# Optimization experiments

Measured on AMD Instinct MI355X. Metric: run time of the kernel, lower is better.

Reference implementation:

```python
import jax, jax.numpy as jnp
import numpy as np
import math

DIM = 2048; H = 16; QR = 1536; KVR = 512; DN = 128; DR = 64; DV = 128
BS = 4; S = 1024
QK_HEAD = DN + DR  # 192


def _rms(x, w, eps=1e-6):
    v = jnp.mean(x * x, axis=-1, keepdims=True)
    return w * (x * jax.lax.rsqrt(v + eps))


def _rope_cos_sin(seq_len, dim):
    inv_freq = 1.0 / (10000.0 ** (jnp.arange(0, dim, 2, dtype=jnp.float32) / dim))
    t = jnp.arange(seq_len, dtype=jnp.float32)
    freqs = jnp.einsum('s,d->sd', t, inv_freq)
    freqs = jnp.concatenate([freqs, freqs], axis=-1)  # [S, dim]
    return jnp.cos(freqs), jnp.sin(freqs)


def _rotate_half(x):
    x1, x2 = jnp.split(x, 2, axis=-1)
    return jnp.concatenate([-x2, x1], axis=-1)


def setup_inputs() -> dict:
    key = jax.random.key(0)
    ks = jax.random.split(key, 12)
    sd = 0.02
    x = jax.random.normal(ks[0], (BS, S, DIM), dtype=jnp.float32)
    # causal additive mask [b, s, t]
    i = jnp.arange(S)
    causal = jnp.where(i[:, None] >= i[None, :], 0.0, -1e9).astype(jnp.float32)
    mask = jnp.broadcast_to(causal, (BS, S, S))
    return {
        'x': x,
        'mask': mask,
        'wq_a_w': jax.random.normal(ks[1], (QR, DIM)) * sd,
        'wq_a_b': jnp.zeros((QR,), jnp.float32),
        'q_norm_w': jnp.ones((QR,), jnp.float32),
        'wq_b_w': jax.random.normal(ks[2], (H * QK_HEAD, QR)) * sd,
        'wq_b_b': jnp.zeros((H * QK_HEAD,), jnp.float32),
        'wkv_a_w': jax.random.normal(ks[3], (KVR + DR, DIM)) * sd,
        'wkv_a_b': jnp.zeros((KVR + DR,), jnp.float32),
        'kv_norm_w': jnp.ones((KVR,), jnp.float32),
        'wkv_b_w': jax.random.normal(ks[4], (H * (DN + DV), KVR)) * sd,
        'wo_w': jax.random.normal(ks[5], (DIM, H * DV)) * sd,
        'wo_b': jnp.zeros((DIM,), jnp.float32),
    }


def reference(x, mask, wq_a_w, wq_a_b, q_norm_w, wq_b_w, wq_b_b,
              wkv_a_w, wkv_a_b, kv_norm_w, wkv_b_w, wo_w, wo_b):
    bs, seq_len, _ = x.shape
    # Q low-rank path
    q = x @ wq_a_w.T + wq_a_b                     # [b,s,QR]
    q = _rms(q, q_norm_w)
    q = q @ wq_b_w.T + wq_b_b                     # [b,s,H*192]
    q = q.reshape(bs, seq_len, H, QK_HEAD)
    q_nope, q_pe = q[..., :DN], q[..., DN:]       # [b,s,h,128], [b,s,h,64]
    # compressed KV path
    kv = x @ wkv_a_w.T + wkv_a_b                  # [b,s,KVR+64]
    c, k_pe = kv[..., :KVR], kv[..., KVR:]        # [b,s,512], [b,s,64]
    # RoPE on the rope sub-dims
    cos, sin = _rope_cos_sin(seq_len, DR)         # [s,64]
    cos4 = cos[None, :, None, :]
    sin4 = sin[None, :, None, :]
    q_pe = q_pe * cos4 + _rotate_half(q_pe) * sin4
    k_pe4 = k_pe[:, :, None, :]
    k_pe = (k_pe4 * cos4 + _rotate_half(k_pe4) * sin4)[:, :, 0, :]  # [b,s,64]
    # weight absorption: wkv_b viewed [H, DN+DV, KVR]
    wkv_b = wkv_b_w.reshape(H, DN + DV, KVR)
    q_abs = jnp.einsum('bshd,hdc->bshc', q_nope, wkv_b[:, :DN])      # [b,s,h,512]
    c_n = _rms(c, kv_norm_w)                                         # [b,t,512]
    scores = (jnp.einsum('bshc,btc->bsht', q_abs, c_n)
              + jnp.einsum('bshr,btr->bsht', q_pe, k_pe)) / math.sqrt(QK_HEAD)
    scores = scores + mask[:, :, None, :]
    scores = jax.nn.softmax(scores, axis=-1)
    o = jnp.einsum('bsht,btc->bshc', scores, c_n)                    # [b,s,h,512]
    o = jnp.einsum('bshc,hdc->bshd', o, wkv_b[:, -DV:])              # [b,s,h,128]
    o = o.reshape(bs, seq_len, H * DV)
    return o @ wo_w.T + wo_b
```

## Files before the change

### kernel.cpp

```cpp
#include <hip/hip_runtime.h>


typedef __attribute__((ext_vector_type(8))) short bf16x8;
typedef __attribute__((ext_vector_type(4))) float f32x4;
typedef __attribute__((ext_vector_type(4))) int i32x4;
typedef unsigned short ushort_t;
typedef unsigned int uint32;

typedef const __attribute__((address_space(1))) void* gas_ptr;
typedef __attribute__((address_space(3))) void* las_ptr;

#define DEV __device__ __forceinline__
#define WAITVM(N) asm volatile("s_waitcnt vmcnt(" #N ")" ::: "memory")

DEV float b2f(ushort_t u) { return __uint_as_float(((uint32)u) << 16); }
DEV ushort_t f2b(float f) {
  uint32 u = __float_as_uint(f);
  return (ushort_t)((u + 0x7fffu + ((u >> 16) & 1u)) >> 16);
}
DEV uint32 pkb(float lo, float hi) { return (uint32)f2b(lo) | ((uint32)f2b(hi) << 16); }

DEV void c4seg(const float4* __restrict__ in, ushort4* __restrict__ out, int i, int n4) {
  if (i < n4) {
    float4 v = in[i];
    ushort4 o; o.x = f2b(v.x); o.y = f2b(v.y); o.z = f2b(v.z); o.w = f2b(v.w);
    out[i] = o;
  }
}
DEV void vbseg(const float* __restrict__ in, ushort_t* __restrict__ out, int i4, int dofs) {
  int c4 = i4 & 127, d = (i4 >> 7) & 127, h = i4 >> 14;
  const float4 v = *(const float4*)(in + ((long)(h * 256 + dofs + d)) * 512 + c4 * 4);
  ushort4 o; o.x = f2b(v.x); o.y = f2b(v.y); o.z = f2b(v.z); o.w = f2b(v.w);
  ((ushort4*)out)[i4] = o;
}
__global__ __launch_bounds__(256) void castall_k(
    const float* __restrict__ x, const float* __restrict__ wq_a_w,
    const float* __restrict__ wkv_a_w, const float* __restrict__ wq_b_w,
    const float* __restrict__ wo_w, const float* __restrict__ wkv_b_w,
    ushort_t* __restrict__ xb, ushort_t* __restrict__ wcomb,
    ushort_t* __restrict__ wqb, ushort_t* __restrict__ wo,
    ushort_t* __restrict__ wkvbv, ushort_t* __restrict__ wkvbn) {
  int blk = blockIdx.x, tid = threadIdx.x;
  if (blk < 8192) {
    c4seg((const float4*)x, (ushort4*)xb, blk * 256 + tid, 2097152);
  } else if (blk < 11264) {
    c4seg((const float4*)wq_a_w, (ushort4*)wcomb, (blk - 8192) * 256 + tid, 786432);
  } else if (blk < 12416) {
    c4seg((const float4*)wkv_a_w, (ushort4*)(wcomb + 1536 * 2048),
          (blk - 11264) * 256 + tid, 294912);
  } else if (blk < 17024) {
    c4seg((const float4*)wq_b_w, (ushort4*)wqb, (blk - 12416) * 256 + tid, 1179648);
  } else if (blk < 21120) {
    c4seg((const float4*)wo_w, (ushort4*)wo, (blk - 17024) * 256 + tid, 1048576);
  } else if (blk < 22144) {
    vbseg(wkv_b_w, wkvbv, (blk - 21120) * 256 + tid, 128);
  } else {
    vbseg(wkv_b_w, wkvbn, (blk - 22144) * 256 + tid, 0);
  }
}

DEV float block_reduce_sum(float v, float* sbuf) {
#pragma unroll
  for (int d = 32; d >= 1; d >>= 1) v += __shfl_xor(v, d);
  if ((threadIdx.x & 63) == 0) sbuf[threadIdx.x >> 6] = v;
  __syncthreads();
  return sbuf[0] + sbuf[1] + sbuf[2] + sbuf[3];
}

__global__ __launch_bounds__(256) void rms_1536_k(const float* __restrict__ in,
                                                  ushort_t* __restrict__ out,
                                                  const float* __restrict__ w) {
  __shared__ float sbuf[4];
  long row = blockIdx.x;
  const float* p = in + row * 1536;
  float v[6]; float ss = 0.f;
#pragma unroll
  for (int i = 0; i < 6; ++i) { v[i] = p[threadIdx.x + i * 256]; ss += v[i] * v[i]; }
  ss = block_reduce_sum(ss, sbuf);
  float sc = rsqrtf(ss * (1.0f / 1536.0f) + 1e-6f);
#pragma unroll
  for (int i = 0; i < 6; ++i) {
    int c = threadIdx.x + i * 256;
    out[row * 1536 + c] = f2b(v[i] * sc * w[c]);
  }
}

__global__ __launch_bounds__(512) void kvfuse_k(const float* __restrict__ kvf,
                                                const float* __restrict__ w,
                                                ushort_t* __restrict__ kcat,
                                                ushort_t* __restrict__ vtp,
                                                ushort_t* __restrict__ kabs) {
  __shared__ ushort_t sh[8 * 512];
  int tid = threadIdx.x, wv = tid >> 6, lane = tid & 63;
  long row = (long)blockIdx.x * 8 + wv;
  const float* p = kvf + row * 576;
  float4 v0 = *(const float4*)(p + lane * 8);
  float4 v1 = *(const float4*)(p + lane * 8 + 4);
  float ss = v0.x * v0.x + v0.y * v0.y + v0.z * v0.z + v0.w * v0.w
           + v1.x * v1.x + v1.y * v1.y + v1.z * v1.z + v1.w * v1.w;
#pragma unroll
  for (int d = 1; d <= 32; d <<= 1) ss += __shfl_xor(ss, d);
  float sc = rsqrtf(ss * (1.0f / 512.0f) + 1e-6f);
  float4 w0 = *(const float4*)(w + lane * 8);
  float4 w1 = *(const float4*)(w + lane * 8 + 4);
  ushort_t tmp[8];
  tmp[0] = f2b(v0.x * sc * w0.x); tmp[1] = f2b(v0.y * sc * w0.y);
  tmp[2] = f2b(v0.z * sc * w0.z); tmp[3] = f2b(v0.w * sc * w0.w);
  tmp[4] = f2b(v1.x * sc * w1.x); tmp[5] = f2b(v1.y * sc * w1.y);
  tmp[6] = f2b(v1.z * sc * w1.z); tmp[7] = f2b(v1.w * sc * w1.w);
  *(uint4*)(kcat + row * 576 + lane * 8) = *(uint4*)tmp;
  *(uint4*)(sh + wv * 512 + lane * 8) = *(uint4*)tmp;
  if (lane < 32) {
    int t = (int)(row & 1023);
    float x1 = p[512 + lane], x2 = p[544 + lane];
    float ang = (float)t * powf(10000.0f, -(float)lane * (1.0f / 32.0f));
    float s, c; sincosf(ang, &s, &c);
    ushort_t r1 = f2b(x1 * c - x2 * s), r2 = f2b(x2 * c + x1 * s);
    kcat[row * 576 + 512 + lane] = r1;
    kcat[row * 576 + 544 + lane] = r2;
#pragma unroll
    for (int h = 0; h < 16; ++h) {
      long base = ((long)h * 4096 + row) * 192;
      kabs[base + 128 + lane] = r1;
      kabs[base + 160 + lane] = r2;
    }
  }
  __syncthreads();
  ushort_t t8[8];
#pragma unroll
  for (int j = 0; j < 8; ++j) t8[j] = sh[j * 512 + tid];
  int b = blockIdx.x >> 7, tb = blockIdx.x & 127;
  *(uint4*)(vtp + (((long)b * 128 + tb) * 512 + tid) * 8) = *(uint4*)t8;
}

template <bool OUT_BF16>
__global__ __launch_bounds__(256) void gemm_bt_k(
    const ushort_t* __restrict__ A, int lda, long sAz,
    const ushort_t* __restrict__ B, int ldb, long sBz,
    void* __restrict__ C, int ldc, long sCz,
    const float* __restrict__ bias, float scale,
    int M, int N, int K) {
  __shared__ ushort_t As[2 * 4096];
  __shared__ ushort_t Bs[2 * 4096];
  int tid = threadIdx.x;
  int wave = tid >> 6, lane = tid & 63;
  int row0 = blockIdx.x * 128, col0 = blockIdx.y * 128;
  int z = blockIdx.z;
  const ushort_t* Az = A + (long)z * sAz;
  const ushort_t* Bz = B + (long)z * sBz;
  int wr = wave >> 1, wc = wave & 1;
  int lr = lane & 15, kq = lane >> 4;

  f32x4 acc[4][4];
#pragma unroll
  for (int m = 0; m < 4; ++m)
#pragma unroll
    for (int n = 0; n < 4; ++n) acc[m][n] = (f32x4){0.f, 0.f, 0.f, 0.f};

  auto stage = [&](int buf, int k0) {
#pragma unroll
    for (int rnd = 0; rnd < 2; ++rnd) {
      int e = rnd * 2048 + wave * 512 + lane * 8;
      int tr = e >> 5, tc = e & 31;
      int ar = row0 + tr; if (ar >= M) ar = M - 1;
      int br = col0 + tr; if (br >= N) br = N - 1;
      __builtin_amdgcn_global_load_lds((gas_ptr)(Az + (long)ar * lda + (k0 + tc)),
          (las_ptr)(As + buf * 4096 + rnd * 2048 + wave * 512), 16, 0, 0);
      __builtin_amdgcn_global_load_lds((gas_ptr)(Bz + (long)br * ldb + (k0 + tc)),
          (las_ptr)(Bs + buf * 4096 + rnd * 2048 + wave * 512), 16, 0, 0);
    }
  };

  stage(0, 0);
  int nk = K >> 5;
  for (int kt = 0; kt < nk; ++kt) {
    int cur = kt & 1;
    if (kt + 1 < nk) { stage(cur ^ 1, (kt + 1) * 32); WAITVM(4); }
    else { WAITVM(0); }
    __builtin_amdgcn_s_barrier();
    __builtin_amdgcn_sched_barrier(0);
    const ushort_t* Ac = As + cur * 4096;
    const ushort_t* Bc = Bs + cur * 4096;
    bf16x8 a[4], bb[4];
#pragma unroll
    for (int m = 0; m < 4; ++m)
      a[m] = *(const bf16x8*)(Ac + (wr * 64 + m * 16 + lr) * 32 + kq * 8);
#pragma unroll
    for (int n = 0; n < 4; ++n)
      bb[n] = *(const bf16x8*)(Bc + (wc * 64 + n * 16 + lr) * 32 + kq * 8);
#pragma unroll
    for (int m = 0; m < 4; ++m)
#pragma unroll
      for (int n = 0; n < 4; ++n)
        acc[m][n] = __builtin_amdgcn_mfma_f32_16x16x32_bf16(a[m], bb[n], acc[m][n], 0, 0, 0);
    __builtin_amdgcn_s_barrier();
  }

#pragma unroll
  for (int n = 0; n < 4; ++n) {
    int gcol = col0 + wc * 64 + n * 16 + lr;
    if (gcol >= N) continue;
    float bv = bias ? bias[gcol] : 0.f;
#pragma unroll
    for (int m = 0; m < 4; ++m) {
      int gr0 = row0 + wr * 64 + m * 16 + kq * 4;
#pragma unroll
      for (int r = 0; r < 4; ++r) {
        int gr = gr0 + r;
        if (gr < M) {
          float v = acc[m][n][r] * scale + bv;
          long ci = (long)z * sCz + (long)gr * ldc + gcol;
          if constexpr (OUT_BF16) ((ushort_t*)C)[ci] = f2b(v);
          else ((float*)C)[ci] = v;
        }
      }
    }
  }
}

template <int MODE>
__global__ __launch_bounds__(256) void gemm64_k(
    const ushort_t* __restrict__ A, int lda,
    const ushort_t* __restrict__ B, int ldb,
    void* __restrict__ C, int ldc,
    const float* __restrict__ bias,
    void* __restrict__ C2, const float* __restrict__ bias2,
    int M, int N, int K) {
  __shared__ ushort_t As[2 * 8192];
  __shared__ ushort_t Bs[2 * 8192];
  int tid = threadIdx.x;
  int wave = tid >> 6, lane = tid & 63;
  int row0 = blockIdx.x * 128, col0 = blockIdx.y * 128;
  int wr = wave >> 1, wc = wave & 1;
  int lr = lane & 15, kq = lane >> 4;
  int rsw = lr & 7;

  f32x4 acc[4][4];
#pragma unroll
  for (int m = 0; m < 4; ++m)
#pragma unroll
    for (int n = 0; n < 4; ++n) acc[m][n] = (f32x4){0.f, 0.f, 0.f, 0.f};

  auto stage = [&](int buf, int k0) {
#pragma unroll
    for (int ii = 0; ii < 4; ++ii) {
      int e = ii * 256 + tid;
      int r = e >> 3, c = e & 7;
      int scol = ((c ^ (r & 7)) << 3);
      int ar = row0 + r; if (ar >= M) ar = M - 1;
      int br = col0 + r; if (br >= N) br = N - 1;
      __builtin_amdgcn_global_load_lds((gas_ptr)(A + (long)ar * lda + k0 + scol),
          (las_ptr)(As + buf * 8192 + e * 8), 16, 0, 0);
      __builtin_amdgcn_global_load_lds((gas_ptr)(B + (long)br * ldb + k0 + scol),
          (las_ptr)(Bs + buf * 8192 + e * 8), 16, 0, 0);
    }
  };

  stage(0, 0);
  int nk = K >> 6;
  for (int kt = 0; kt < nk; ++kt) {
    int cur = kt & 1;
    if (kt + 1 < nk) { stage(cur ^ 1, (kt + 1) * 64); WAITVM(8); }
    else { WAITVM(0); }
    __builtin_amdgcn_s_barrier();
    __builtin_amdgcn_sched_barrier(0);
    const ushort_t* Ac = As + cur * 8192;
    const ushort_t* Bc = Bs + cur * 8192;
#pragma unroll
    for (int ks = 0; ks < 2; ++ks) {
      bf16x8 a[4], bb[4];
#pragma unroll
      for (int m = 0; m < 4; ++m) {
        int row = wr * 64 + m * 16 + lr;
        a[m] = *(const bf16x8*)(Ac + row * 64 + ((((ks << 2) | kq) ^ rsw) << 3));
      }
#pragma unroll
      for (int n = 0; n < 4; ++n) {
        int row = wc * 64 + n * 16 + lr;
        bb[n] = *(const bf16x8*)(Bc + row * 64 + ((((ks << 2) | kq) ^ rsw) << 3));
      }
#pragma unroll
      for (int m = 0; m < 4; ++m)
#pragma unroll
        for (int n = 0; n < 4; ++n)
          acc[m][n] = __builtin_amdgcn_mfma_f32_16x16x32_bf16(a[m], bb[n], acc[m][n], 0, 0, 0);
    }
    __builtin_amdgcn_s_barrier();
  }

  if constexpr (MODE == 0) {
#pragma unroll
    for (int n = 0; n < 4; ++n) {
      int gcol = col0 + wc * 64 + n * 16 + lr;
      if (gcol >= N) continue;
      float bv = bias[gcol];
#pragma unroll
      for (int m = 0; m < 4; ++m) {
        int gr0 = row0 + wr * 64 + m * 16 + kq * 4;
#pragma unroll
        for (int r = 0; r < 4; ++r) {
          int gr = gr0 + r;
          if (gr < M) ((float*)C)[(long)gr * ldc + gcol] = acc[m][n][r] + bv;
        }
      }
    }
  } else if constexpr (MODE == 1) {
#pragma unroll
    for (int n = 0; n < 4; ++n) {
      int gcol = col0 + wc * 64 + n * 16 + lr;
      if (gcol >= N) continue;
      if (gcol < 1536) {
        float bv = bias[gcol];
#pragma unroll
        for (int m = 0; m < 4; ++m) {
          int gr0 = row0 + wr * 64 + m * 16 + kq * 4;
#pragma unroll
          for (int r = 0; r < 4; ++r) {
            int gr = gr0 + r;
            ((float*)C)[(long)gr * 1536 + gcol] = acc[m][n][r] + bv;
          }
        }
      } else {
        int c2 = gcol - 1536;
        float bv = bias2[c2];
#pragma unroll
        for (int m = 0; m < 4; ++m) {
          int gr0 = row0 + wr * 64 + m * 16 + kq * 4;
#pragma unroll
          for (int r = 0; r < 4; ++r) {
            int gr = gr0 + r;
            ((float*)C2)[(long)gr * 576 + c2] = acc[m][n][r] + bv;
          }
        }
      }
    }
  } else {
    const float RS = 0.07216878364870322f;
    ushort_t* qc = (ushort_t*)C;
#pragma unroll
    for (int n = 0; n < 4; ++n) {
      int j = col0 + wc * 64 + n * 16 + lr;
      int h = j / 192, d = j - h * 192;
      if (d < 128) {
        float bv = bias[j];
#pragma unroll
        for (int m = 0; m < 4; ++m) {
          int gr0 = row0 + wr * 64 + m * 16 + kq * 4;
#pragma unroll
          for (int r = 0; r < 4; ++r) {
            int gr = gr0 + r;
            qc[((long)h * 4096 + gr) * 192 + d] = f2b((acc[m][n][r] + bv) * RS);
          }
        }
      } else if (d < 160) {
        int jj = d - 128;
        float bv1 = bias[j], bv2 = bias[j + 32];
        float invf = powf(10000.0f, -(float)jj * (1.0f / 32.0f));
#pragma unroll
        for (int m = 0; m < 4; ++m) {
          int gr0 = row0 + wr * 64 + m * 16 + kq * 4;
#pragma unroll
          for (int r = 0; r < 4; ++r) {
            int gr = gr0 + r;
            int t = gr & 1023;
            float s, c; sincosf((float)t * invf, &s, &c);
            float x1 = acc[m][n][r] + bv1;
            float x2 = acc[m][n + 2][r] + bv2;
            long base = ((long)h * 4096 + gr) * 192;
            qc[base + d] = f2b((x1 * c - x2 * s) * RS);
            qc[base + d + 32] = f2b((x2 * c + x1 * s) * RS);
          }
        }
      }
    }
  }
}

__global__ __launch_bounds__(512, 1) void flash5_k(const ushort_t* __restrict__ qcat2,
                                                   const ushort_t* __restrict__ kabs,
                                                   const ushort_t* __restrict__ vtp,
                                                   ushort_t* __restrict__ O) {
  __shared__ __align__(16) ushort_t SMEM[2 * 6400 + 2 * 16384];

  int tid = threadIdx.x;
  int wave = tid >> 6, lane = tid & 63;
  int lr = lane & 15, kq = lane >> 4;
  int bi = blockIdx.x;
  int jz = bi >> 6;
  int qb = (jz < 4) ? jz : 11 - jz;
  int bh = bi & 63;
  int h = bh >> 2, b = bh & 3;
  int s0 = qb * 128;
  int nt = (qb + 1) * 4;

  const ushort_t* kt = kabs + ((long)h * 4096 + b * 1024) * 192;
  const ushort_t* vt = vtp + (long)b * 524288;
  const ushort_t* qp = qcat2 + ((long)(h * 4096 + b * 1024 + s0 + wave * 16 + lr)) * 192 + kq * 8;

  auto stageK = [&](int buf, int t0) {
    const ushort_t* sb = kt + (long)t0 * 192;
    ushort_t* kb = SMEM + buf * 6400;
#pragma unroll
    for (int ii = 0; ii < 2; ++ii) {
      int c = ii * 512 + tid;
      if (ii == 1 && tid >= 288) break;
      int t = (int)((unsigned)c / 25u);
      int r = c - t * 25;
      int rr = (r == 24) ? 0 : r;
      const ushort_t* src = sb + t * 192 + rr * 8;
      __builtin_amdgcn_global_load_lds((gas_ptr)src, (las_ptr)(kb + c * 8), 16, 0, 0);
    }
  };
  auto stageV = [&](int buf, int t0) {
    const ushort_t* sb = vt + (long)(t0 >> 3) * 4096;
    ushort_t* vb = SMEM + 12800 + buf * 16384;
#pragma unroll
    for (int ii = 0; ii < 4; ++ii) {
      int c0 = (ii * 8 + wave) * 64;
      const ushort_t* src = sb + (long)(c0 + lane) * 8;
      __builtin_amdgcn_global_load_lds((gas_ptr)src, (las_ptr)(vb + c0 * 8), 16, 0, 0);
    }
  };

  stageK(0, 0); stageV(0, 0);
  bf16x8 qreg[6];
#pragma unroll
  for (int st = 0; st < 6; ++st) qreg[st] = *(const bf16x8*)(qp + st * 32);

  f32x4 o[32];
#pragma unroll
  for (int v = 0; v < 32; ++v) o[v] = (f32x4){0.f, 0.f, 0.f, 0.f};
  float m_run = -1e30f, l_run = 0.f;

  int row_g = s0 + wave * 16 + lr;
  int idx_lo = (((kq & 1) << 5) + lr) << 2;
  int idx_hi = idx_lo + 64;
  bool losel = (kq < 2);

  __syncthreads();

  for (int it = 0; it < nt; ++it) {
    int cur = it & 1;
    if (it + 1 < nt) { stageK(cur ^ 1, (it + 1) * 32); stageV(cur ^ 1, (it + 1) * 32); }
    const ushort_t* Kc = SMEM + cur * 6400;
    f32x4 sv0 = (f32x4){0.f, 0.f, 0.f, 0.f}, sv1 = sv0;
    __builtin_amdgcn_s_setprio(1);
#pragma unroll
    for (int st = 0; st < 6; ++st) {
      int off = st * 32 + kq * 8;
      bf16x8 k0 = *(const bf16x8*)(Kc + lr * 200 + off);
      bf16x8 k1 = *(const bf16x8*)(Kc + (16 + lr) * 200 + off);
      sv0 = __builtin_amdgcn_mfma_f32_16x16x32_bf16(k0, qreg[st], sv0, 0, 0, 0);
      sv1 = __builtin_amdgcn_mfma_f32_16x16x32_bf16(k1, qreg[st], sv1, 0, 0, 0);
    }
    __builtin_amdgcn_s_setprio(0);
    int t0 = it * 32;
    if (t0 >= s0) {
#pragma unroll
      for (int rr = 0; rr < 4; ++rr) {
        if (t0 + kq * 4 + rr > row_g) sv0[rr] = -1e30f;
        if (t0 + 16 + kq * 4 + rr > row_g) sv1[rr] = -1e30f;
      }
    }
    float mx = fmaxf(fmaxf(fmaxf(sv0[0], sv0[1]), fmaxf(sv0[2], sv0[3])),
                     fmaxf(fmaxf(sv1[0], sv1[1]), fmaxf(sv1[2], sv1[3])));
    mx = fmaxf(mx, __shfl_xor(mx, 16));
    mx = fmaxf(mx, __shfl_xor(mx, 32));
    float mn = (mx > m_run + 8.0f) ? mx : m_run;
    float alpha = __expf(m_run - mn);
    float p0 = __expf(sv0[0] - mn), p1 = __expf(sv0[1] - mn);
    float p2 = __expf(sv0[2] - mn), p3 = __expf(sv0[3] - mn);
    float p4 = __expf(sv1[0] - mn), p5 = __expf(sv1[1] - mn);
    float p6 = __expf(sv1[2] - mn), p7 = __expf(sv1[3] - mn);
    float psum = ((p0 + p1) + (p2 + p3)) + ((p4 + p5) + (p6 + p7));
    psum += __shfl_xor(psum, 16);
    psum += __shfl_xor(psum, 32);
    l_run = l_run * alpha + psum;
    m_run = mn;
    int u0 = (int)pkb(p0, p1), u1 = (int)pkb(p2, p3);
    int u2 = (int)pkb(p4, p5), u3 = (int)pkb(p6, p7);
    int b00 = __builtin_amdgcn_ds_bpermute(idx_lo, u0);
    int b10 = __builtin_amdgcn_ds_bpermute(idx_lo, u1);
    int b20 = __builtin_amdgcn_ds_bpermute(idx_lo, u2);
    int b30 = __builtin_amdgcn_ds_bpermute(idx_lo, u3);
    int b01 = __builtin_amdgcn_ds_bpermute(idx_hi, u0);
    int b11 = __builtin_amdgcn_ds_bpermute(idx_hi, u1);
    int b21 = __builtin_amdgcn_ds_bpermute(idx_hi, u2);
    int b31 = __builtin_amdgcn_ds_bpermute(idx_hi, u3);
    i32x4 w;
    w.x = losel ? b00 : b20; w.y = losel ? b10 : b30;
    w.z = losel ? b01 : b21; w.w = losel ? b11 : b31;
    bf16x8 pa = __builtin_bit_cast(bf16x8, w);
    float a0 = __shfl(alpha, kq * 4 + 0), a1 = __shfl(alpha, kq * 4 + 1);
    float a2 = __shfl(alpha, kq * 4 + 2), a3 = __shfl(alpha, kq * 4 + 3);
    if (__any((a0 != 1.f) | (a1 != 1.f) | (a2 != 1.f) | (a3 != 1.f))) {
      f32x4 av; av[0] = a0; av[1] = a1; av[2] = a2; av[3] = a3;
#pragma unroll
      for (int v = 0; v < 32; ++v) o[v] *= av;
    }
    const ushort_t* Vc = SMEM + 12800 + cur * 16384 + (kq * 512 + lr) * 8;
    __builtin_amdgcn_s_setprio(1);
#pragma unroll
    for (int v = 0; v < 32; ++v) {
      bf16x8 bv = *(const bf16x8*)(Vc + v * 128);
      o[v] = __builtin_amdgcn_mfma_f32_16x16x32_bf16(pa, bv, o[v], 0, 0, 0);
    }
    __builtin_amdgcn_s_setprio(0);
    __syncthreads();
  }
  float l0 = __shfl(l_run, kq * 4 + 0), l1 = __shfl(l_run, kq * 4 + 1);
  float l2 = __shfl(l_run, kq * 4 + 2), l3 = __shfl(l_run, kq * 4 + 3);
  f32x4 inv; inv[0] = 1.f / l0; inv[1] = 1.f / l1; inv[2] = 1.f / l2; inv[3] = 1.f / l3;
  ushort_t* ob = O + ((long)(h * 4096 + b * 1024 + s0 + wave * 16 + kq * 4)) * 512 + lr;
#pragma unroll
  for (int rr = 0; rr < 4; ++rr) {
    ushort_t* orow = ob + (long)rr * 512;
#pragma unroll
    for (int v = 0; v < 32; ++v) orow[v * 16] = f2b(o[v][rr] * inv[rr]);
  }
}

extern "C" void kernel_launch(void* const* d_in, const int* in_sizes, int n_in,
                              void* d_out, int out_size, void* d_ws, size_t ws_size,
                              hipStream_t stream) {
  (void)in_sizes; (void)n_in;
  const float* x         = (const float*)d_in[0];
  const float* wq_a_w    = (const float*)d_in[2];
  const float* wq_a_b    = (const float*)d_in[3];
  const float* q_norm_w  = (const float*)d_in[4];
  const float* wq_b_w    = (const float*)d_in[5];
  const float* wq_b_b    = (const float*)d_in[6];
  const float* wkv_a_w   = (const float*)d_in[7];
  const float* wkv_a_b   = (const float*)d_in[8];
  const float* kv_norm_w = (const float*)d_in[9];
  const float* wkv_b_w   = (const float*)d_in[10];
  const float* wo_w      = (const float*)d_in[11];
  const float* wo_b      = (const float*)d_in[12];

  char* ws = (char*)d_ws;
  constexpr size_t OFF_XB     = 0;
  constexpr size_t OFF_WCOMB  = 16777216;
  constexpr size_t OFF_WQB    = 25427968;
  constexpr size_t OFF_QA     = 34865152;
  constexpr size_t OFF_QAN    = 60030976;
  constexpr size_t OFF_QCAT2  = 72613888;
  constexpr size_t OFF_WKVBN  = 97779712;
  constexpr size_t OFF_WKVBV  = 99876864;
  constexpr size_t OFF_WO     = 101974016;
  constexpr size_t OFF_KVF    = 110362624;
  constexpr size_t OFF_KCAT   = 119799808;
  constexpr size_t OFF_VTP    = 124518400;
  constexpr size_t OFF_KABS   = 128712704;
  constexpr size_t OFF_O      = 153878528;
  constexpr size_t OFF_O2     = 220987392;
  constexpr size_t WS_NEED    = 237764608;
  if (ws_size < WS_NEED) {
    (void)hipMemsetAsync(d_out, 0, (size_t)out_size * sizeof(float), stream);
    return;
  }

  ushort_t* xb     = (ushort_t*)(ws + OFF_XB);
  ushort_t* wcomb  = (ushort_t*)(ws + OFF_WCOMB);
  ushort_t* wqb    = (ushort_t*)(ws + OFF_WQB);
  float*    qa     = (float*)(ws + OFF_QA);
  ushort_t* qan    = (ushort_t*)(ws + OFF_QAN);
  ushort_t* qcat2  = (ushort_t*)(ws + OFF_QCAT2);
  ushort_t* wkvbn  = (ushort_t*)(ws + OFF_WKVBN);
  ushort_t* wkvbv  = (ushort_t*)(ws + OFF_WKVBV);
  ushort_t* wo     = (ushort_t*)(ws + OFF_WO);
  float*    kvf    = (float*)(ws + OFF_KVF);
  ushort_t* kcat   = (ushort_t*)(ws + OFF_KCAT);
  ushort_t* vtp    = (ushort_t*)(ws + OFF_VTP);
  ushort_t* kabs   = (ushort_t*)(ws + OFF_KABS);
  ushort_t* Obuf   = (ushort_t*)(ws + OFF_O);
  ushort_t* o2     = (ushort_t*)(ws + OFF_O2);

  castall_k<<<23168, 256, 0, stream>>>(x, wq_a_w, wkv_a_w, wq_b_w, wo_w, wkv_b_w,
                                       xb, wcomb, wqb, wo, wkvbv, wkvbn);
  gemm64_k<1><<<dim3(32, 17), 256, 0, stream>>>(xb, 2048, wcomb, 2048,
      qa, 1536, wq_a_b, kvf, wkv_a_b, 4096, 2112, 2048);
  rms_1536_k<<<4096, 256, 0, stream>>>(qa, qan, q_norm_w);
  gemm64_k<2><<<dim3(32, 24), 256, 0, stream>>>(qan, 1536, wqb, 1536,
      qcat2, 0, wq_b_b, nullptr, nullptr, 4096, 3072, 1536);
  kvfuse_k<<<512, 512, 0, stream>>>(kvf, kv_norm_w, kcat, vtp, kabs);
  gemm_bt_k<true><<<dim3(32, 1, 16), 256, 0, stream>>>(kcat, 576, 0,
      wkvbn, 512, (long)128 * 512, kabs, 192, (long)4096 * 192,
      nullptr, 1.f, 4096, 128, 512);
  flash5_k<<<512, 512, 0, stream>>>(qcat2, kabs, vtp, Obuf);
  gemm_bt_k<true><<<dim3(32, 1, 16), 256, 0, stream>>>(Obuf, 512, (long)4096 * 512,
      wkvbv, 512, (long)128 * 512, o2, 2048, 128, nullptr, 1.f, 4096, 128, 512);
  gemm64_k<0><<<dim3(32, 16), 256, 0, stream>>>(o2, 2048, wo, 2048,
      (float*)d_out, 2048, wo_b, nullptr, nullptr, 4096, 2048, 2048);
}
```

Baseline: 386.5 us.

## Transpose MFMA operands for vectorized epilogue stores and swizzle GEMM block order

The MFMA operands are swapped in both GEMM kernels, so each lane now holds four consecutive columns of one row instead of four rows of one column. The epilogues then write 16-byte float4 or 8-byte packed bf16 vectors in place of scalar strided stores, with the RoPE branch adapted to match. The 128x128 GEMM also remaps block indices with a stride-8 swizzle, meant to improve L2 reuse between concurrently running blocks. This relies on N being a multiple of 4 and the grid size divisible by 8 for a complete mapping. In the RoPE path, n>=2 lanes with d0 in the 128..160 range would use nn=0, which looks fragile.

```diff
diff --git a/kernel.cpp b/kernel.cpp
--- a/kernel.cpp
+++ b/kernel.cpp
@@ -192,27 +192,27 @@
     for (int m = 0; m < 4; ++m)
 #pragma unroll
       for (int n = 0; n < 4; ++n)
-        acc[m][n] = __builtin_amdgcn_mfma_f32_16x16x32_bf16(a[m], bb[n], acc[m][n], 0, 0, 0);
+        acc[m][n] = __builtin_amdgcn_mfma_f32_16x16x32_bf16(bb[n], a[m], acc[m][n], 0, 0, 0);
     __builtin_amdgcn_s_barrier();
   }
 
 #pragma unroll
-  for (int n = 0; n < 4; ++n) {
-    int gcol = col0 + wc * 64 + n * 16 + lr;
-    if (gcol >= N) continue;
-    float bv = bias ? bias[gcol] : 0.f;
-#pragma unroll
-    for (int m = 0; m < 4; ++m) {
-      int gr0 = row0 + wr * 64 + m * 16 + kq * 4;
-#pragma unroll
-      for (int r = 0; r < 4; ++r) {
-        int gr = gr0 + r;
-        if (gr < M) {
-          float v = acc[m][n][r] * scale + bv;
-          long ci = (long)z * sCz + (long)gr * ldc + gcol;
-          if constexpr (OUT_BF16) ((ushort_t*)C)[ci] = f2b(v);
-          else ((float*)C)[ci] = v;
-        }
+  for (int m = 0; m < 4; ++m) {
+    int gr = row0 + wr * 64 + m * 16 + lr;
+    if (gr >= M) continue;
+#pragma unroll
+    for (int n = 0; n < 4; ++n) {
+      int cb = col0 + wc * 64 + n * 16 + kq * 4;
+      if (cb >= N) continue;
+      f32x4 v = acc[m][n];
+#pragma unroll
+      for (int r = 0; r < 4; ++r) v[r] = v[r] * scale + (bias ? bias[cb + r] : 0.f);
+      long ci = (long)z * sCz + (long)gr * ldc + cb;
+      if constexpr (OUT_BF16) {
+        ushort4 pk; pk.x = f2b(v[0]); pk.y = f2b(v[1]); pk.z = f2b(v[2]); pk.w = f2b(v[3]);
+        *(ushort4*)((ushort_t*)C + ci) = pk;
+      } else {
+        *(f32x4*)((float*)C + ci) = v;
       }
     }
   }
@@ -230,7 +230,11 @@
   __shared__ ushort_t Bs[2 * 8192];
   int tid = threadIdx.x;
   int wave = tid >> 6, lane = tid & 63;
-  int row0 = blockIdx.x * 128, col0 = blockIdx.y * 128;
+  int bid = blockIdx.y * gridDim.x + blockIdx.x;
+  int nwg = gridDim.x * gridDim.y;
+  int swz = (bid & 7) * (nwg >> 3) + (bid >> 3);
+  int bx = swz % gridDim.x, by = swz / gridDim.x;
+  int row0 = bx * 128, col0 = by * 128;
   int wr = wave >> 1, wc = wave & 1;
   int lr = lane & 15, kq = lane >> 4;
   int rsw = lr & 7;
@@ -283,93 +287,91 @@
       for (int m = 0; m < 4; ++m)
 #pragma unroll
         for (int n = 0; n < 4; ++n)
-          acc[m][n] = __builtin_amdgcn_mfma_f32_16x16x32_bf16(a[m], bb[n], acc[m][n], 0, 0, 0);
+          acc[m][n] = __builtin_amdgcn_mfma_f32_16x16x32_bf16(bb[n], a[m], acc[m][n], 0, 0, 0);
     }
     __builtin_amdgcn_s_barrier();
   }
 
   if constexpr (MODE == 0) {
 #pragma unroll
-    for (int n = 0; n < 4; ++n) {
-      int gcol = col0 + wc * 64 + n * 16 + lr;
-      if (gcol >= N) continue;
-      float bv = bias[gcol];
-#pragma unroll
-      for (int m = 0; m < 4; ++m) {
-        int gr0 = row0 + wr * 64 + m * 16 + kq * 4;
-#pragma unroll
-        for (int r = 0; r < 4; ++r) {
-          int gr = gr0 + r;
-          if (gr < M) ((float*)C)[(long)gr * ldc + gcol] = acc[m][n][r] + bv;
-        }
+    for (int m = 0; m < 4; ++m) {
+      int gr = row0 + wr * 64 + m * 16 + lr;
+      if (gr >= M) continue;
+#pragma unroll
+      for (int n = 0; n < 4; ++n) {
+        int cb = col0 + wc * 64 + n * 16 + kq * 4;
+        if (cb >= N) continue;
+        f32x4 v = acc[m][n];
+#pragma unroll
+        for (int r = 0; r < 4; ++r) v[r] += bias[cb + r];
+        *(f32x4*)((float*)C + (long)gr * ldc + cb) = v;
       }
     }
   } else if constexpr (MODE == 1) {
 #pragma unroll
-    for (int n = 0; n < 4; ++n) {
-      int gcol = col0 + wc * 64 + n * 16 + lr;
-      if (gcol >= N) continue;
-      if (gcol < 1536) {
-        float bv = bias[gcol];
-#pragma unroll
-        for (int m = 0; m < 4; ++m) {
-          int gr0 = row0 + wr * 64 + m * 16 + kq * 4;
-#pragma unroll
-          for (int r = 0; r < 4; ++r) {
-            int gr = gr0 + r;
-            ((float*)C)[(long)gr * 1536 + gcol] = acc[m][n][r] + bv;
-          }
-        }
-      } else {
-        int c2 = gcol - 1536;
-        float bv = bias2[c2];
-#pragma unroll
-        for (int m = 0; m < 4; ++m) {
-          int gr0 = row0 + wr * 64 + m * 16 + kq * 4;
-#pragma unroll
-          for (int r = 0; r < 4; ++r) {
-            int gr = gr0 + r;
-            ((float*)C2)[(long)gr * 576 + c2] = acc[m][n][r] + bv;
-          }
+    for (int m = 0; m < 4; ++m) {
+      int gr = row0 + wr * 64 + m * 16 + lr;
+      if (gr >= M) continue;
+#pragma unroll
+      for (int n = 0; n < 4; ++n) {
+        int cb = col0 + wc * 64 + n * 16 + kq * 4;
+        if (cb >= N) continue;
+        f32x4 v = acc[m][n];
+        if (cb < 1536) {
+#pragma unroll
+          for (int r = 0; r < 4; ++r) v[r] += bias[cb + r];
+          *(f32x4*)((float*)C + (long)gr * 1536 + cb) = v;
+        } else {
+          int c2 = cb - 1536;
+#pragma unroll
+          for (int r = 0; r < 4; ++r) v[r] += bias2[c2 + r];
+          *(f32x4*)((float*)C2 + (long)gr * 576 + c2) = v;
         }
       }
     }
   } else {
     const float RS = 0.07216878364870322f;
-    ushort_t* qc = (ushort_t*)C;
 #pragma unroll
     for (int n = 0; n < 4; ++n) {
-      int j = col0 + wc * 64 + n * 16 + lr;
-      int h = j / 192, d = j - h * 192;
-      if (d < 128) {
-        float bv = bias[j];
+      int cb = col0 + wc * 64 + n * 16 + kq * 4;
+      int h = cb / 192, d0 = cb - h * 192;
+      ushort_t* qh = (ushort_t*)C + (long)h * 4096 * 192;
+      if (d0 < 128) {
+        f32x4 bv; 
+#pragma unroll
+        for (int r = 0; r < 4; ++r) bv[r] = bias[cb + r];
 #pragma unroll
         for (int m = 0; m < 4; ++m) {
-          int gr0 = row0 + wr * 64 + m * 16 + kq * 4;
+          int gr = row0 + wr * 64 + m * 16 + lr;
+          f32x4 v = acc[m][n];
+          ushort4 pk;
+          pk.x = f2b((v[0] + bv[0]) * RS); pk.y = f2b((v[1] + bv[1]) * RS);
+          pk.z = f2b((v[2] + bv[2]) * RS); pk.w = f2b((v[3] + bv[3]) * RS);
+          *(ushort4*)(qh + (long)gr * 192 + d0) = pk;
+        }
+      } else if (d0 < 160) {
+        int nn = (n < 2) ? n : 0;
+        f32x4 bv1, bv2, invf;
+#pragma unroll
+        for (int r = 0; r < 4; ++r) {
+          bv1[r] = bias[cb + r]; bv2[r] = bias[cb + 32 + r];
+          invf[r] = powf(10000.0f, -(float)(d0 - 128 + r) * (1.0f / 32.0f));
+        }
+#pragma unroll
+        for (int m = 0; m < 4; ++m) {
+          int gr = row0 + wr * 64 + m * 16 + lr;
+          int t = gr & 1023;
+          f32x4 v1 = acc[m][nn], v2 = acc[m][nn + 2];
+          ushort4 p1, p2;
 #pragma unroll
           for (int r = 0; r < 4; ++r) {
-            int gr = gr0 + r;
-            qc[((long)h * 4096 + gr) * 192 + d] = f2b((acc[m][n][r] + bv) * RS);
+            float s, c; sincosf((float)t * invf[r], &s, &c);
+            float x1 = v1[r] + bv1[r], x2 = v2[r] + bv2[r];
+            ((ushort_t*)&p1)[r] = f2b((x1 * c - x2 * s) * RS);
+            ((ushort_t*)&p2)[r] = f2b((x2 * c + x1 * s) * RS);
           }
-        }
-      } else if (d < 160) {
-        int jj = d - 128;
-        float bv1 = bias[j], bv2 = bias[j + 32];
-        float invf = powf(10000.0f, -(float)jj * (1.0f / 32.0f));
-#pragma unroll
-        for (int m = 0; m < 4; ++m) {
-          int gr0 = row0 + wr * 64 + m * 16 + kq * 4;
-#pragma unroll
-          for (int r = 0; r < 4; ++r) {
-            int gr = gr0 + r;
-            int t = gr & 1023;
-            float s, c; sincosf((float)t * invf, &s, &c);
-            float x1 = acc[m][n][r] + bv1;
-            float x2 = acc[m][n + 2][r] + bv2;
-            long base = ((long)h * 4096 + gr) * 192;
-            qc[base + d] = f2b((x1 * c - x2 * s) * RS);
-            qc[base + d + 32] = f2b((x2 * c + x1 * s) * RS);
-          }
+          *(ushort4*)(qh + (long)gr * 192 + d0) = p1;
+          *(ushort4*)(qh + (long)gr * 192 + d0 + 32) = p2;
         }
       }
     }
```

Measured after the change: 378.8 us. 1.02x faster.
